# Performance work log

Hardware: AMD Instinct MI355X
Metric: run time of the kernel (lower is better)

The kernel has to match this reference:

```python
import jax, jax.numpy as jnp
import numpy as np

N = 100000   # nodes
E = 1600000  # edges
D = 128      # feature dim
G = 64       # graphs in batch


def setup_inputs() -> dict:
    key = jax.random.key(0)
    k1, k2, k3, k4, k5, k6, k7, k8 = jax.random.split(key, 8)
    in_feat = jax.random.normal(k1, (N, D), dtype=jnp.float32)
    src = jax.random.randint(k2, (E,), 0, N, dtype=jnp.int32)
    dst = jax.random.randint(k3, (E,), 0, N, dtype=jnp.int32)
    graph_ids = jax.random.randint(k4, (N,), 0, G, dtype=jnp.int32)
    s = 1.0 / np.sqrt(D)
    W1 = jax.random.uniform(k5, (D, D), jnp.float32, -s, s)
    b1 = jnp.zeros((D,), jnp.float32)
    W2 = jax.random.uniform(k6, (D, D), jnp.float32, -s, s)
    b2 = jnp.zeros((D,), jnp.float32)
    return {"in_feat": in_feat, "W1": W1, "b1": b1, "W2": W2, "b2": b2,
            "src": src, "dst": dst, "graph_ids": graph_ids}


def _graph_conv(x, src, dst, W, b, norm_src, norm_dst):
    # DGL GraphConv, norm='both': D_out^{-1/2} A D_in^{-1/2} X W + b
    m = (x * norm_src[:, None])[src]                       # [E, d] gather
    agg = jax.ops.segment_sum(m, dst, num_segments=N)      # [N, d] scatter-add
    return (agg * norm_dst[:, None]) @ W + b


def reference(in_feat, W1, b1, W2, b2, src, dst, graph_ids):
    ones_e = jnp.ones((E,), jnp.float32)
    deg_out = jax.ops.segment_sum(ones_e, src, num_segments=N)
    deg_in = jax.ops.segment_sum(ones_e, dst, num_segments=N)
    norm_src = jnp.where(deg_out > 0, deg_out, 1.0) ** -0.5  # D_out^{-1/2}
    norm_dst = jnp.where(deg_in > 0, deg_in, 1.0) ** -0.5    # D_in^{-1/2}

    h = _graph_conv(in_feat, src, dst, W1, b1, norm_src, norm_dst)
    h = jax.nn.relu(h)
    h = _graph_conv(h, src, dst, W2, b2, norm_src, norm_dst)

    # AvgPooling: per-graph mean over nodes -> [G, D]
    sums = jax.ops.segment_sum(h, graph_ids, num_segments=G)
    counts = jax.ops.segment_sum(jnp.ones((N,), jnp.float32), graph_ids, num_segments=G)
    return sums / jnp.maximum(counts, 1.0)[:, None]
```

## Files before the change

kernel.cpp:

```cpp
#include <hip/hip_runtime.h>
#include <cstdint>


#define DD 128
#define PB 512
#define GB 384
#define KC 32
#define CHK 3200

typedef __attribute__((ext_vector_type(8))) short bf16x8;
typedef __attribute__((ext_vector_type(4))) float f32x4;
typedef __attribute__((ext_vector_type(2))) float f32x2;

__device__ __forceinline__ unsigned short f2bf(float f) {
  union { float f; unsigned u; } v; v.f = f;
  unsigned r = (v.u + 0x7fff + ((v.u >> 16) & 1)) >> 16;
  return (unsigned short)r;
}
__device__ __forceinline__ float bfhi(unsigned u) {
  union { unsigned u; float f; } v; v.u = u & 0xffff0000u; return v.f;
}
__device__ __forceinline__ float bflo(unsigned u) {
  union { unsigned u; float f; } v; v.u = u << 16; return v.f;
}
__device__ __forceinline__ unsigned char f2fp8(float f) {
  return (unsigned char)(__builtin_amdgcn_cvt_pk_fp8_f32(f, f, 0, false) & 0xff);
}

__global__ __launch_bounds__(256) void k_part1a(const int* __restrict__ src, const int* __restrict__ dst,
                                                const int* __restrict__ gid,
                                                unsigned* __restrict__ histD, unsigned* __restrict__ histS,
                                                int* __restrict__ gcnt, int E, int N, int G) {
  __shared__ unsigned hD[256], hS[256];
  __shared__ int h64[64];
  hD[threadIdx.x] = 0; hS[threadIdx.x] = 0;
  if (threadIdx.x < 64) h64[threadIdx.x] = 0;
  __syncthreads();
  int chunk = (E + gridDim.x - 1) / gridDim.x;
  int e0 = blockIdx.x * chunk, e1 = min(E, e0 + chunk);
  for (int e = e0 + threadIdx.x; e < e1; e += 256) {
    atomicAdd(&hD[(unsigned)dst[e] >> 9], 1u);
    atomicAdd(&hS[(unsigned)src[e] >> 9], 1u);
  }
  int stride = gridDim.x * 256;
  for (int i = blockIdx.x * 256 + threadIdx.x; i < N; i += stride)
    atomicAdd(&h64[gid[i]], 1);
  __syncthreads();
  histD[blockIdx.x * 256 + threadIdx.x] = hD[threadIdx.x];
  histS[blockIdx.x * 256 + threadIdx.x] = hS[threadIdx.x];
  if (threadIdx.x < (unsigned)G) {
    int v = h64[threadIdx.x];
    if (v) atomicAdd(&gcnt[threadIdx.x], v);
  }
}

__global__ __launch_bounds__(256) void k_pscanA(unsigned* __restrict__ histD, unsigned* __restrict__ histS,
                                                unsigned* __restrict__ tot) {
  __shared__ unsigned excl[PB], psc[256];
  int table = blockIdx.x >> 8, b = blockIdx.x & 255;
  unsigned* hist = table ? histS : histD;
  int t = threadIdx.x;
  unsigned s0 = hist[(2 * t) * 256 + b];
  unsigned s1 = hist[(2 * t + 1) * 256 + b];
  unsigned pr = s0 + s1;
  psc[t] = pr;
  __syncthreads();
  for (int off = 1; off < 256; off <<= 1) {
    unsigned x = (t >= off) ? psc[t - off] : 0;
    __syncthreads();
    psc[t] += x;
    __syncthreads();
  }
  unsigned pex = psc[t] - pr;
  excl[2 * t] = pex;
  excl[2 * t + 1] = pex + s0;
  __syncthreads();
  hist[(2 * t) * 256 + b] = excl[2 * t];
  hist[(2 * t + 1) * 256 + b] = excl[2 * t + 1];
  if (t == 255) tot[table * 256 + b] = psc[255];
}

__global__ __launch_bounds__(256) void k_pscanB(const unsigned* __restrict__ tot,
                                                int* __restrict__ bsD, int* __restrict__ bsS) {
  __shared__ unsigned s[256];
  int t = threadIdx.x;
#pragma unroll
  for (int table = 0; table < 2; ++table) {
    int* bs = table ? bsS : bsD;
    unsigned v = tot[table * 256 + t];
    s[t] = v;
    __syncthreads();
    for (int off = 1; off < 256; off <<= 1) {
      unsigned x = (t >= off) ? s[t - off] : 0;
      __syncthreads();
      s[t] += x;
      __syncthreads();
    }
    bs[t] = (int)(s[t] - v);
    if (t == 255) bs[256] = (int)s[255];
    __syncthreads();
  }
}

__global__ __launch_bounds__(256) void k_pscanC(unsigned* __restrict__ histD, unsigned* __restrict__ histS,
                                                const int* __restrict__ bsD, const int* __restrict__ bsS) {
  int table = blockIdx.x >> 9, i = blockIdx.x & (PB - 1);
  unsigned* hist = table ? histS : histD;
  const int* bs = table ? bsS : bsD;
  hist[i * 256 + threadIdx.x] += (unsigned)bs[threadIdx.x];
}

__global__ __launch_bounds__(256) void k_part1c(const int* __restrict__ src, const int* __restrict__ dst,
                                                const unsigned* __restrict__ histD, const unsigned* __restrict__ histS,
                                                unsigned* __restrict__ pairD, unsigned* __restrict__ pairS, int E) {
  __shared__ unsigned pk[CHK];
  __shared__ unsigned char bk[CHK];
  __shared__ unsigned hist[256], cur[256], gbase[256], psc[256];
  int chunk = (E + gridDim.x - 1) / gridDim.x;
  int e0 = blockIdx.x * chunk, e1 = min(E, e0 + chunk);
  int n = e1 - e0;
  int t = threadIdx.x;
#pragma unroll
  for (int table = 0; table < 2; ++table) {
    const unsigned* gcur = (table ? histS : histD) + blockIdx.x * 256;
    unsigned* out = table ? pairS : pairD;
    hist[t] = 0;
    __syncthreads();
    for (int i = t; i < n; i += 256) {
      unsigned key = (unsigned)(table ? src[e0 + i] : dst[e0 + i]);
      atomicAdd(&hist[key >> 9], 1u);
    }
    __syncthreads();
    unsigned v = hist[t];
    psc[t] = v;
    __syncthreads();
    for (int off = 1; off < 256; off <<= 1) {
      unsigned x = (t >= off) ? psc[t - off] : 0;
      __syncthreads();
      psc[t] += x;
      __syncthreads();
    }
    unsigned excl = psc[t] - v;
    cur[t] = excl;
    gbase[t] = gcur[t] - excl;
    __syncthreads();
    for (int i = t; i < n; i += 256) {
      unsigned sv = (unsigned)src[e0 + i], dv = (unsigned)dst[e0 + i];
      unsigned key = table ? sv : dv;
      unsigned val = table ? (((sv & 511u) << 17) | dv) : (((dv & 511u) << 17) | sv);
      unsigned b = key >> 9;
      unsigned p = atomicAdd(&cur[b], 1u);
      pk[p] = val;
      bk[p] = (unsigned char)b;
    }
    __syncthreads();
    for (int i = t; i < n; i += 256)
      out[gbase[bk[i]] + i] = pk[i];
    __syncthreads();
  }
}

__global__ __launch_bounds__(256) void k_part2d(const unsigned* __restrict__ pairD, const int* __restrict__ bsD,
                                                int* __restrict__ offs, int* __restrict__ degI,
                                                int* __restrict__ srcS, int N) {
  __shared__ unsigned hist[512], excl[512], psc[256];
  int k = blockIdx.x, base = k << 9;
  int b0 = bsD[k], b1 = bsD[k + 1];
  hist[threadIdx.x] = 0; hist[threadIdx.x + 256] = 0;
  __syncthreads();
  for (int i = b0 + threadIdx.x; i < b1; i += 256)
    atomicAdd(&hist[pairD[i] >> 17], 1u);
  __syncthreads();
  unsigned s0 = hist[2 * threadIdx.x], s1 = hist[2 * threadIdx.x + 1];
  unsigned pr = s0 + s1;
  psc[threadIdx.x] = pr;
  __syncthreads();
  for (int off = 1; off < 256; off <<= 1) {
    unsigned x = (threadIdx.x >= off) ? psc[threadIdx.x - off] : 0;
    __syncthreads();
    psc[threadIdx.x] += x;
    __syncthreads();
  }
  unsigned pex = psc[threadIdx.x] - pr;
  excl[2 * threadIdx.x] = pex;
  excl[2 * threadIdx.x + 1] = pex + s0;
  __syncthreads();
  for (int j = threadIdx.x; j < 512; j += 256) {
    int node = base + j;
    if (node <= N) offs[node] = b0 + (int)excl[j];
    if (node < N) degI[node] = (int)hist[j];
  }
  __syncthreads();
  for (int i = b0 + threadIdx.x; i < b1; i += 256) {
    unsigned pkv = pairD[i];
    unsigned pos = atomicAdd(&excl[pkv >> 17], 1u);
    srcS[b0 + (int)pos] = (int)(pkv & 0x1FFFFu);
  }
}

__global__ __launch_bounds__(256) void k_norm(const int* __restrict__ degI, const int* __restrict__ gcnt,
                                              const int* __restrict__ gid,
                                              float* __restrict__ ndst, uint2* __restrict__ pwg, int N) {
  int i = blockIdx.x * blockDim.x + threadIdx.x;
  if (i >= N) return;
  float gi = (float)degI[i]; gi = gi > 0.f ? gi : 1.f;
  float nd = rsqrtf(gi);
  ndst[i] = nd;
  float c = (float)gcnt[gid[i]]; c = c > 1.f ? c : 1.f;
  float w = nd / c;
  union { float f; unsigned u; } v; v.f = w;
  pwg[i] = make_uint2(v.u, (unsigned)gid[i]);
}

__global__ __launch_bounds__(1024, 1) void k_pw(const unsigned* __restrict__ pairS, const int* __restrict__ bsS,
                                                const uint2* __restrict__ pwg,
                                                unsigned short* __restrict__ P16,
                                                float* __restrict__ nsrc, int N) {
  __shared__ float tile[512 * 64];
  __shared__ unsigned hist[512];
  int k = blockIdx.x, base = k << 9;
  int b0 = bsS[k], b1 = bsS[k + 1];
  for (int i = threadIdx.x; i < 512 * 64; i += 1024) tile[i] = 0.f;
  if (threadIdx.x < 512) hist[threadIdx.x] = 0;
  __syncthreads();
  for (int i = b0 + threadIdx.x; i < b1; i += 1024) {
    unsigned pkv = pairS[i];
    unsigned dv = pkv & 0x1FFFFu;
    unsigned sloc = pkv >> 17;
    atomicAdd(&hist[sloc], 1u);
    uint2 u = pwg[dv];
    union { unsigned u; float f; } w; w.u = u.x;
    atomicAdd(&tile[sloc * 64 + u.y], w.f);
  }
  __syncthreads();
  if (threadIdx.x < 512) {
    int node = base + threadIdx.x;
    if (node < N) {
      float g = (float)hist[threadIdx.x]; g = g > 0.f ? g : 1.f;
      nsrc[node] = rsqrtf(g);
    }
  }
  for (int grp = threadIdx.x; grp < 4096; grp += 1024) {
    int qb = grp >> 6, g = grp & 63;
    unsigned w0 = (unsigned)f2bf(tile[(qb * 8 + 0) * 64 + g]) | ((unsigned)f2bf(tile[(qb * 8 + 1) * 64 + g]) << 16);
    unsigned w1 = (unsigned)f2bf(tile[(qb * 8 + 2) * 64 + g]) | ((unsigned)f2bf(tile[(qb * 8 + 3) * 64 + g]) << 16);
    unsigned w2 = (unsigned)f2bf(tile[(qb * 8 + 4) * 64 + g]) | ((unsigned)f2bf(tile[(qb * 8 + 5) * 64 + g]) << 16);
    unsigned w3 = (unsigned)f2bf(tile[(qb * 8 + 6) * 64 + g]) | ((unsigned)f2bf(tile[(qb * 8 + 7) * 64 + g]) << 16);
    uint4 o = make_uint4(w0, w1, w2, w3);
    *(uint4*)(P16 + ((size_t)(base >> 3) + qb) * 512 + g * 8) = o;
  }
}

__global__ __launch_bounds__(128) void k_wprep(const float* __restrict__ W, unsigned short* __restrict__ Wt) {
  int n = blockIdx.x, k = threadIdx.x;
  Wt[n * 128 + k] = f2bf(W[k * 128 + n]);
}

__global__ __launch_bounds__(256) void k_gemm1(const float* __restrict__ X, const unsigned short* __restrict__ Wt,
                                               const float* __restrict__ nsrc,
                                               unsigned char* __restrict__ Z8, int N) {
  int wave = threadIdx.x >> 6, lane = threadIdx.x & 63;
  int quad = lane >> 4, l16 = lane & 15;
  int row0 = blockIdx.x * 64 + wave * 16;
  int arow = row0 + l16; if (arow >= N) arow = N - 1;
  const float* xr = X + (size_t)arow * 128 + quad * 8;
  f32x4 acc[8];
#pragma unroll
  for (int i = 0; i < 8; ++i) acc[i] = (f32x4){0.f, 0.f, 0.f, 0.f};
#pragma unroll
  for (int kb = 0; kb < 128; kb += 32) {
    float4 x0 = *(const float4*)(xr + kb);
    float4 x1 = *(const float4*)(xr + kb + 4);
    bf16x8 a;
    a[0] = (short)f2bf(x0.x); a[1] = (short)f2bf(x0.y);
    a[2] = (short)f2bf(x0.z); a[3] = (short)f2bf(x0.w);
    a[4] = (short)f2bf(x1.x); a[5] = (short)f2bf(x1.y);
    a[6] = (short)f2bf(x1.z); a[7] = (short)f2bf(x1.w);
#pragma unroll
    for (int nt = 0; nt < 8; ++nt) {
      bf16x8 b = *(const bf16x8*)(Wt + (size_t)(nt * 16 + l16) * 128 + kb + quad * 8);
      acc[nt] = __builtin_amdgcn_mfma_f32_16x16x32_bf16(a, b, acc[nt], 0, 0, 0);
    }
  }
  int rbase = row0 + quad * 4;
#pragma unroll
  for (int r = 0; r < 4; ++r) {
    int row = rbase + r;
    if (row < N) {
      float s = nsrc[row];
#pragma unroll
      for (int nt = 0; nt < 8; ++nt)
        Z8[(size_t)row * 128 + nt * 16 + l16] = f2fp8(acc[nt][r] * s);
    }
  }
}

#define ACCP(u) do {                                              \
    c0 += __builtin_amdgcn_cvt_pk_f32_fp8((u).x, false);          \
    c1 += __builtin_amdgcn_cvt_pk_f32_fp8((u).x, true);           \
    c2 += __builtin_amdgcn_cvt_pk_f32_fp8((u).y, false);          \
    c3 += __builtin_amdgcn_cvt_pk_f32_fp8((u).y, true);           \
  } while (0)

__global__ __launch_bounds__(256) void k_layer1(const unsigned char* __restrict__ Z8,
                                                const int* __restrict__ offs, const int* __restrict__ srcS,
                                                const float* __restrict__ b1,
                                                const float* __restrict__ nsrc, const float* __restrict__ ndst,
                                                unsigned short* __restrict__ Hb, int N) {
  int lane = threadIdx.x & 63;
  int q = lane >> 4, l16 = lane & 15;
  int d = blockIdx.x * 16 + (threadIdx.x >> 6) * 4 + q;
  bool live = d < N;
  int dc = live ? d : N - 1;
  int start = offs[dc];
  int end = live ? offs[dc + 1] : start;
  const int boff = l16 * 8;
  const unsigned char* zb = Z8 + boff;
  float4 bv0 = *(const float4*)(b1 + boff);
  float4 bv1 = *(const float4*)(b1 + boff + 4);
  float nd = ndst[dc], ns = nsrc[dc];
  f32x2 c0 = {0.f, 0.f}, c1 = {0.f, 0.f}, c2 = {0.f, 0.f}, c3 = {0.f, 0.f};
  int e = start;
  int rem = end - start;
  int s0 = (rem > 0) ? srcS[e] : 0;
  int s1 = (rem > 1) ? srcS[e + 1] : 0;
  while (__any(rem > 0)) {
    uint2 u0 = make_uint2(0u, 0u), u1 = make_uint2(0u, 0u);
    if (rem > 0) u0 = *(const uint2*)(zb + ((size_t)s0 << 7));
    if (rem > 1) u1 = *(const uint2*)(zb + ((size_t)s1 << 7));
    int rem2 = rem - 2;
    if (rem2 > 0) {
      s0 = srcS[e + 2];
      if (rem2 > 1) s1 = srcS[e + 3];
    }
    ACCP(u0);
    ACCP(u1);
    e += 2;
    rem = rem2;
  }
  if (live) {
    float h0 = fmaxf(fmaf(nd, c0[0], bv0.x), 0.f) * ns;
    float h1 = fmaxf(fmaf(nd, c0[1], bv0.y), 0.f) * ns;
    float h2 = fmaxf(fmaf(nd, c1[0], bv0.z), 0.f) * ns;
    float h3 = fmaxf(fmaf(nd, c1[1], bv0.w), 0.f) * ns;
    float h4 = fmaxf(fmaf(nd, c2[0], bv1.x), 0.f) * ns;
    float h5 = fmaxf(fmaf(nd, c2[1], bv1.y), 0.f) * ns;
    float h6 = fmaxf(fmaf(nd, c3[0], bv1.z), 0.f) * ns;
    float h7 = fmaxf(fmaf(nd, c3[1], bv1.w), 0.f) * ns;
    unsigned w0 = (unsigned)f2bf(h0) | ((unsigned)f2bf(h1) << 16);
    unsigned w1 = (unsigned)f2bf(h2) | ((unsigned)f2bf(h3) << 16);
    unsigned w2 = (unsigned)f2bf(h4) | ((unsigned)f2bf(h5) << 16);
    unsigned w3 = (unsigned)f2bf(h6) | ((unsigned)f2bf(h7) << 16);
    *(uint4*)(Hb + (size_t)d * 128 + boff) = make_uint4(w0, w1, w2, w3);
  }
}

__global__ __launch_bounds__(256) void k_poolgemm(const unsigned short* __restrict__ P16,
                                                  const unsigned short* __restrict__ Hb,
                                                  float* __restrict__ part, int N, int Kpad, int chunk) {
  __shared__ unsigned short Hl[KC * 128];
  int t = threadIdx.x;
  int r0 = blockIdx.x * chunk;
  int r1 = min(Kpad, r0 + chunk);
  int wv = t >> 6, lane = t & 63, quad = lane >> 4, l16 = lane & 15;
  f32x4 acc[8];
#pragma unroll
  for (int i = 0; i < 8; ++i) acc[i] = (f32x4){0.f, 0.f, 0.f, 0.f};
  for (int rb = r0; rb < r1; rb += KC) {
    int r = t >> 3, c = (t & 7) * 16;
    int cs = c ^ ((r >> 3) * 16);
    int row = rb + r;
    if (row < N) {
      const uint4* srcp = (const uint4*)(Hb + (size_t)row * 128 + c);
      *(uint4*)(Hl + r * 128 + cs) = srcp[0];
      *(uint4*)(Hl + r * 128 + cs + 8) = srcp[1];
    } else {
      uint4 z = make_uint4(0, 0, 0, 0);
      *(uint4*)(Hl + r * 128 + cs) = z;
      *(uint4*)(Hl + r * 128 + cs + 8) = z;
    }
    __syncthreads();
    bf16x8 a = *(const bf16x8*)(P16 + ((size_t)(rb >> 3) + quad) * 512 + (wv * 16 + l16) * 8);
#pragma unroll
    for (int ft = 0; ft < 8; ++ft) {
      bf16x8 b;
#pragma unroll
      for (int j = 0; j < 8; ++j) {
        int rr = quad * 8 + j;
        b[j] = (short)Hl[rr * 128 + ((ft ^ (rr >> 3)) * 16) + l16];
      }
      acc[ft] = __builtin_amdgcn_mfma_f32_16x16x32_bf16(a, b, acc[ft], 0, 0, 0);
    }
    __syncthreads();
  }
  float* bp = part + (size_t)blockIdx.x * 64 * DD;
#pragma unroll
  for (int ft = 0; ft < 8; ++ft)
#pragma unroll
    for (int rg = 0; rg < 4; ++rg)
      bp[(wv * 16 + quad * 4 + rg) * DD + ft * 16 + l16] = acc[ft][rg];
}

__global__ __launch_bounds__(256) void k_fold(const float* __restrict__ part, float* __restrict__ pooled) {
  int tid = blockIdx.x * 256 + threadIdx.x;
  int o = tid & 8191, grp = tid >> 13;
  float s = 0.f;
  for (int k = grp; k < GB; k += 8) s += part[(size_t)k * 8192 + o];
  unsafeAtomicAdd(&pooled[o], s);
}

__global__ __launch_bounds__(128) void k_out(const float* __restrict__ pooled, const float* __restrict__ W2,
                                             const float* __restrict__ b2, float* __restrict__ out) {
  __shared__ float p[DD];
  int g = blockIdx.x, d = threadIdx.x;
  p[d] = pooled[g * DD + d];
  __syncthreads();
  float a = b2[d];
#pragma unroll 4
  for (int k = 0; k < DD; ++k) a = fmaf(p[k], W2[k * DD + d], a);
  out[g * DD + d] = a;
}

extern "C" void kernel_launch(void* const* d_in, const int* in_sizes, int n_in,
                              void* d_out, int out_size, void* d_ws, size_t ws_size,
                              hipStream_t stream) {
  const float* X  = (const float*)d_in[0];
  const float* W1 = (const float*)d_in[1];
  const float* b1 = (const float*)d_in[2];
  const float* W2 = (const float*)d_in[3];
  const float* b2 = (const float*)d_in[4];
  const int* src  = (const int*)d_in[5];
  const int* dst  = (const int*)d_in[6];
  const int* gid  = (const int*)d_in[7];
  int E = in_sizes[5];
  int N = in_sizes[7];
  int G = out_size / DD;
  int nb = (N >> 9) + 1;
  int Kpad = nb << 9;
  int chunk = ((Kpad + GB * KC - 1) / (GB * KC)) * KC;

  char* w = (char*)d_ws;
  size_t o = 0;
  auto carve = [&](size_t bytes) { char* p = w + o; o += (bytes + 255) & ~(size_t)255; return p; };
  int*   gcnt   = (int*)  carve((size_t)G * 4);
  float* pooled = (float*)carve((size_t)G * DD * 4);
  size_t zeroBytes = o;
  unsigned* histD = (unsigned*)carve((size_t)PB * 256 * 4);
  unsigned* histS = (unsigned*)carve((size_t)PB * 256 * 4);
  unsigned* tot   = (unsigned*)carve(512 * 4);
  int*   bsD    = (int*)  carve(257 * 4);
  int*   bsS    = (int*)  carve(257 * 4);
  unsigned* pairD = (unsigned*)carve((size_t)E * 4);
  unsigned* pairS = (unsigned*)carve((size_t)E * 4);
  int*   srcS   = (int*)  carve((size_t)E * 4);
  int*   offs   = (int*)  carve((size_t)(N + 1) * 4);
  int*   degI   = (int*)  carve((size_t)N * 4);
  float* nsrc   = (float*)carve((size_t)N * 4);
  float* ndst   = (float*)carve((size_t)N * 4);
  uint2* pwg    = (uint2*)carve((size_t)N * 8);
  unsigned short* Wt = (unsigned short*)carve(128 * 128 * 2);
  unsigned char*  Z8 = (unsigned char*)carve((size_t)N * DD);
  unsigned short* Hb = (unsigned short*)carve((size_t)N * DD * 2);
  unsigned short* P16 = (unsigned short*)carve((size_t)Kpad * 64 * 2);
  float* part   = (float*)pairD;

  hipMemsetAsync(d_ws, 0, zeroBytes, stream);

  k_part1a<<<PB, 256, 0, stream>>>(src, dst, gid, histD, histS, gcnt, E, N, G);
  k_pscanA<<<512, 256, 0, stream>>>(histD, histS, tot);
  k_pscanB<<<1, 256, 0, stream>>>(tot, bsD, bsS);
  k_pscanC<<<2 * PB, 256, 0, stream>>>(histD, histS, bsD, bsS);
  k_part1c<<<PB, 256, 0, stream>>>(src, dst, histD, histS, pairD, pairS, E);
  k_part2d<<<nb, 256, 0, stream>>>(pairD, bsD, offs, degI, srcS, N);
  k_norm<<<(N + 255) / 256, 256, 0, stream>>>(degI, gcnt, gid, ndst, pwg, N);
  k_pw<<<nb, 1024, 0, stream>>>(pairS, bsS, pwg, P16, nsrc, N);
  k_wprep<<<128, 128, 0, stream>>>(W1, Wt);
  k_gemm1<<<(N + 63) / 64, 256, 0, stream>>>(X, Wt, nsrc, Z8, N);
  k_layer1<<<(N + 15) / 16, 256, 0, stream>>>(Z8, offs, srcS, b1, nsrc, ndst, Hb, N);
  k_poolgemm<<<GB, 256, 0, stream>>>(P16, Hb, part, N, Kpad, chunk);
  k_fold<<<256, 256, 0, stream>>>(part, pooled);
  k_out<<<G, DD, 0, stream>>>(pooled, W2, b2, (float*)d_out);
}
```

Before: 298.7 us.

## Fuse norm into part2d, merge partition passes, deepen gather prefetch, drop fold kernel

k_part1c now reuses the per-block histograms saved by k_part1a instead of recounting, and scatters both dst- and src-keyed pairs in a single pass over the edges. The separate k_norm kernel is folded into k_part2d, which writes ndst and pwg directly from its local degree histogram. The layer-1 gather loop prefetches four source indices per step instead of two to keep more loads in flight. k_poolgemm atomically adds its partial results straight into pooled, which removes the partial buffer and the k_fold kernel. The costs are two extra histogram arrays, roughly doubled shared memory in k_part1c, and much more atomic traffic onto a small pooled array.

```diff
diff --git a/kernel.cpp b/kernel.cpp
--- a/kernel.cpp
+++ b/kernel.cpp
@@ -17,12 +17,6 @@
   unsigned r = (v.u + 0x7fff + ((v.u >> 16) & 1)) >> 16;
   return (unsigned short)r;
 }
-__device__ __forceinline__ float bfhi(unsigned u) {
-  union { unsigned u; float f; } v; v.u = u & 0xffff0000u; return v.f;
-}
-__device__ __forceinline__ float bflo(unsigned u) {
-  union { unsigned u; float f; } v; v.u = u << 16; return v.f;
-}
 __device__ __forceinline__ unsigned char f2fp8(float f) {
   return (unsigned char)(__builtin_amdgcn_cvt_pk_fp8_f32(f, f, 0, false) & 0xff);
 }
@@ -30,6 +24,7 @@
 __global__ __launch_bounds__(256) void k_part1a(const int* __restrict__ src, const int* __restrict__ dst,
                                                 const int* __restrict__ gid,
                                                 unsigned* __restrict__ histD, unsigned* __restrict__ histS,
+                                                unsigned* __restrict__ rawD, unsigned* __restrict__ rawS,
                                                 int* __restrict__ gcnt, int E, int N, int G) {
   __shared__ unsigned hD[256], hS[256];
   __shared__ int h64[64];
@@ -46,8 +41,11 @@
   for (int i = blockIdx.x * 256 + threadIdx.x; i < N; i += stride)
     atomicAdd(&h64[gid[i]], 1);
   __syncthreads();
-  histD[blockIdx.x * 256 + threadIdx.x] = hD[threadIdx.x];
-  histS[blockIdx.x * 256 + threadIdx.x] = hS[threadIdx.x];
+  unsigned vd = hD[threadIdx.x], vs = hS[threadIdx.x];
+  histD[blockIdx.x * 256 + threadIdx.x] = vd;
+  histS[blockIdx.x * 256 + threadIdx.x] = vs;
+  rawD[blockIdx.x * 256 + threadIdx.x] = vd;
+  rawS[blockIdx.x * 256 + threadIdx.x] = vs;
   if (threadIdx.x < (unsigned)G) {
     int v = h64[threadIdx.x];
     if (v) atomicAdd(&gcnt[threadIdx.x], v);
@@ -112,56 +110,62 @@
 
 __global__ __launch_bounds__(256) void k_part1c(const int* __restrict__ src, const int* __restrict__ dst,
                                                 const unsigned* __restrict__ histD, const unsigned* __restrict__ histS,
+                                                const unsigned* __restrict__ rawD, const unsigned* __restrict__ rawS,
                                                 unsigned* __restrict__ pairD, unsigned* __restrict__ pairS, int E) {
-  __shared__ unsigned pk[CHK];
-  __shared__ unsigned char bk[CHK];
-  __shared__ unsigned hist[256], cur[256], gbase[256], psc[256];
+  __shared__ unsigned pkD[CHK], pkS[CHK];
+  __shared__ unsigned char bkD[CHK], bkS[CHK];
+  __shared__ unsigned curD[256], curS[256], gbD[256], gbS[256], psc[256];
   int chunk = (E + gridDim.x - 1) / gridDim.x;
   int e0 = blockIdx.x * chunk, e1 = min(E, e0 + chunk);
   int n = e1 - e0;
   int t = threadIdx.x;
-#pragma unroll
-  for (int table = 0; table < 2; ++table) {
-    const unsigned* gcur = (table ? histS : histD) + blockIdx.x * 256;
-    unsigned* out = table ? pairS : pairD;
-    hist[t] = 0;
-    __syncthreads();
-    for (int i = t; i < n; i += 256) {
-      unsigned key = (unsigned)(table ? src[e0 + i] : dst[e0 + i]);
-      atomicAdd(&hist[key >> 9], 1u);
-    }
-    __syncthreads();
-    unsigned v = hist[t];
-    psc[t] = v;
-    __syncthreads();
-    for (int off = 1; off < 256; off <<= 1) {
-      unsigned x = (t >= off) ? psc[t - off] : 0;
-      __syncthreads();
-      psc[t] += x;
-      __syncthreads();
-    }
-    unsigned excl = psc[t] - v;
-    cur[t] = excl;
-    gbase[t] = gcur[t] - excl;
-    __syncthreads();
-    for (int i = t; i < n; i += 256) {
-      unsigned sv = (unsigned)src[e0 + i], dv = (unsigned)dst[e0 + i];
-      unsigned key = table ? sv : dv;
-      unsigned val = table ? (((sv & 511u) << 17) | dv) : (((dv & 511u) << 17) | sv);
-      unsigned b = key >> 9;
-      unsigned p = atomicAdd(&cur[b], 1u);
-      pk[p] = val;
-      bk[p] = (unsigned char)b;
-    }
-    __syncthreads();
-    for (int i = t; i < n; i += 256)
-      out[gbase[bk[i]] + i] = pk[i];
-    __syncthreads();
-  }
+  unsigned vD = rawD[blockIdx.x * 256 + t];
+  psc[t] = vD;
+  __syncthreads();
+  for (int off = 1; off < 256; off <<= 1) {
+    unsigned x = (t >= off) ? psc[t - off] : 0;
+    __syncthreads();
+    psc[t] += x;
+    __syncthreads();
+  }
+  unsigned exD = psc[t] - vD;
+  curD[t] = exD;
+  gbD[t] = histD[blockIdx.x * 256 + t] - exD;
+  __syncthreads();
+  unsigned vS = rawS[blockIdx.x * 256 + t];
+  psc[t] = vS;
+  __syncthreads();
+  for (int off = 1; off < 256; off <<= 1) {
+    unsigned x = (t >= off) ? psc[t - off] : 0;
+    __syncthreads();
+    psc[t] += x;
+    __syncthreads();
+  }
+  unsigned exS = psc[t] - vS;
+  curS[t] = exS;
+  gbS[t] = histS[blockIdx.x * 256 + t] - exS;
+  __syncthreads();
+  for (int i = t; i < n; i += 256) {
+    unsigned sv = (unsigned)src[e0 + i], dv = (unsigned)dst[e0 + i];
+    unsigned bD = dv >> 9, bS = sv >> 9;
+    unsigned pD = atomicAdd(&curD[bD], 1u);
+    pkD[pD] = ((dv & 511u) << 17) | sv;
+    bkD[pD] = (unsigned char)bD;
+    unsigned pS = atomicAdd(&curS[bS], 1u);
+    pkS[pS] = ((sv & 511u) << 17) | dv;
+    bkS[pS] = (unsigned char)bS;
+  }
+  __syncthreads();
+  for (int i = t; i < n; i += 256)
+    pairD[gbD[bkD[i]] + i] = pkD[i];
+  for (int i = t; i < n; i += 256)
+    pairS[gbS[bkS[i]] + i] = pkS[i];
 }
 
 __global__ __launch_bounds__(256) void k_part2d(const unsigned* __restrict__ pairD, const int* __restrict__ bsD,
-                                                int* __restrict__ offs, int* __restrict__ degI,
+                                                const int* __restrict__ gcnt, const int* __restrict__ gid,
+                                                int* __restrict__ offs, float* __restrict__ ndst,
+                                                uint2* __restrict__ pwg,
                                                 int* __restrict__ srcS, int N) {
   __shared__ unsigned hist[512], excl[512], psc[256];
   int k = blockIdx.x, base = k << 9;
@@ -188,7 +192,15 @@
   for (int j = threadIdx.x; j < 512; j += 256) {
     int node = base + j;
     if (node <= N) offs[node] = b0 + (int)excl[j];
-    if (node < N) degI[node] = (int)hist[j];
+    if (node < N) {
+      float gi = (float)hist[j]; gi = gi > 0.f ? gi : 1.f;
+      float nd = rsqrtf(gi);
+      ndst[node] = nd;
+      float c = (float)gcnt[gid[node]]; c = c > 1.f ? c : 1.f;
+      float w = nd / c;
+      union { float f; unsigned u; } v; v.f = w;
+      pwg[node] = make_uint2(v.u, (unsigned)gid[node]);
+    }
   }
   __syncthreads();
   for (int i = b0 + threadIdx.x; i < b1; i += 256) {
@@ -196,20 +208,6 @@
     unsigned pos = atomicAdd(&excl[pkv >> 17], 1u);
     srcS[b0 + (int)pos] = (int)(pkv & 0x1FFFFu);
   }
-}
-
-__global__ __launch_bounds__(256) void k_norm(const int* __restrict__ degI, const int* __restrict__ gcnt,
-                                              const int* __restrict__ gid,
-                                              float* __restrict__ ndst, uint2* __restrict__ pwg, int N) {
-  int i = blockIdx.x * blockDim.x + threadIdx.x;
-  if (i >= N) return;
-  float gi = (float)degI[i]; gi = gi > 0.f ? gi : 1.f;
-  float nd = rsqrtf(gi);
-  ndst[i] = nd;
-  float c = (float)gcnt[gid[i]]; c = c > 1.f ? c : 1.f;
-  float w = nd / c;
-  union { float f; unsigned u; } v; v.f = w;
-  pwg[i] = make_uint2(v.u, (unsigned)gid[i]);
 }
 
 __global__ __launch_bounds__(1024, 1) void k_pw(const unsigned* __restrict__ pairS, const int* __restrict__ bsS,
@@ -322,21 +320,28 @@
   f32x2 c0 = {0.f, 0.f}, c1 = {0.f, 0.f}, c2 = {0.f, 0.f}, c3 = {0.f, 0.f};
   int e = start;
   int rem = end - start;
-  int s0 = (rem > 0) ? srcS[e] : 0;
-  int s1 = (rem > 1) ? srcS[e + 1] : 0;
+  int s0 = 0, s1 = 0, s2 = 0, s3 = 0;
+  if (rem > 0) s0 = srcS[e];
+  if (rem > 1) s1 = srcS[e + 1];
+  if (rem > 2) s2 = srcS[e + 2];
+  if (rem > 3) s3 = srcS[e + 3];
   while (__any(rem > 0)) {
     uint2 u0 = make_uint2(0u, 0u), u1 = make_uint2(0u, 0u);
+    uint2 u2 = make_uint2(0u, 0u), u3 = make_uint2(0u, 0u);
     if (rem > 0) u0 = *(const uint2*)(zb + ((size_t)s0 << 7));
     if (rem > 1) u1 = *(const uint2*)(zb + ((size_t)s1 << 7));
-    int rem2 = rem - 2;
-    if (rem2 > 0) {
-      s0 = srcS[e + 2];
-      if (rem2 > 1) s1 = srcS[e + 3];
-    }
+    if (rem > 2) u2 = *(const uint2*)(zb + ((size_t)s2 << 7));
+    if (rem > 3) u3 = *(const uint2*)(zb + ((size_t)s3 << 7));
+    if (rem > 4) s0 = srcS[e + 4];
+    if (rem > 5) s1 = srcS[e + 5];
+    if (rem > 6) s2 = srcS[e + 6];
+    if (rem > 7) s3 = srcS[e + 7];
     ACCP(u0);
     ACCP(u1);
-    e += 2;
-    rem = rem2;
+    ACCP(u2);
+    ACCP(u3);
+    e += 4;
+    rem -= 4;
   }
   if (live) {
     float h0 = fmaxf(fmaf(nd, c0[0], bv0.x), 0.f) * ns;
@@ -357,7 +362,7 @@
 
 __global__ __launch_bounds__(256) void k_poolgemm(const unsigned short* __restrict__ P16,
                                                   const unsigned short* __restrict__ Hb,
-                                                  float* __restrict__ part, int N, int Kpad, int chunk) {
+                                                  float* __restrict__ pooled, int N, int Kpad, int chunk) {
   __shared__ unsigned short Hl[KC * 128];
   int t = threadIdx.x;
   int r0 = blockIdx.x * chunk;
@@ -393,20 +398,11 @@
     }
     __syncthreads();
   }
-  float* bp = part + (size_t)blockIdx.x * 64 * DD;
 #pragma unroll
   for (int ft = 0; ft < 8; ++ft)
 #pragma unroll
     for (int rg = 0; rg < 4; ++rg)
-      bp[(wv * 16 + quad * 4 + rg) * DD + ft * 16 + l16] = acc[ft][rg];
-}
-
-__global__ __launch_bounds__(256) void k_fold(const float* __restrict__ part, float* __restrict__ pooled) {
-  int tid = blockIdx.x * 256 + threadIdx.x;
-  int o = tid & 8191, grp = tid >> 13;
-  float s = 0.f;
-  for (int k = grp; k < GB; k += 8) s += part[(size_t)k * 8192 + o];
-  unsafeAtomicAdd(&pooled[o], s);
+      unsafeAtomicAdd(&pooled[(wv * 16 + quad * 4 + rg) * DD + ft * 16 + l16], acc[ft][rg]);
 }
 
 __global__ __launch_bounds__(128) void k_out(const float* __restrict__ pooled, const float* __restrict__ W2,
@@ -447,6 +443,8 @@
   size_t zeroBytes = o;
   unsigned* histD = (unsigned*)carve((size_t)PB * 256 * 4);
   unsigned* histS = (unsigned*)carve((size_t)PB * 256 * 4);
+  unsigned* rawD  = (unsigned*)carve((size_t)PB * 256 * 4);
+  unsigned* rawS  = (unsigned*)carve((size_t)PB * 256 * 4);
   unsigned* tot   = (unsigned*)carve(512 * 4);
   int*   bsD    = (int*)  carve(257 * 4);
   int*   bsS    = (int*)  carve(257 * 4);
@@ -454,7 +452,6 @@
   unsigned* pairS = (unsigned*)carve((size_t)E * 4);
   int*   srcS   = (int*)  carve((size_t)E * 4);
   int*   offs   = (int*)  carve((size_t)(N + 1) * 4);
-  int*   degI   = (int*)  carve((size_t)N * 4);
   float* nsrc   = (float*)carve((size_t)N * 4);
   float* ndst   = (float*)carve((size_t)N * 4);
   uint2* pwg    = (uint2*)carve((size_t)N * 8);
@@ -462,22 +459,19 @@
   unsigned char*  Z8 = (unsigned char*)carve((size_t)N * DD);
   unsigned short* Hb = (unsigned short*)carve((size_t)N * DD * 2);
   unsigned short* P16 = (unsigned short*)carve((size_t)Kpad * 64 * 2);
-  float* part   = (float*)pairD;
 
   hipMemsetAsync(d_ws, 0, zeroBytes, stream);
 
-  k_part1a<<<PB, 256, 0, stream>>>(src, dst, gid, histD, histS, gcnt, E, N, G);
+  k_part1a<<<PB, 256, 0, stream>>>(src, dst, gid, histD, histS, rawD, rawS, gcnt, E, N, G);
   k_pscanA<<<512, 256, 0, stream>>>(histD, histS, tot);
   k_pscanB<<<1, 256, 0, stream>>>(tot, bsD, bsS);
   k_pscanC<<<2 * PB, 256, 0, stream>>>(histD, histS, bsD, bsS);
-  k_part1c<<<PB, 256, 0, stream>>>(src, dst, histD, histS, pairD, pairS, E);
-  k_part2d<<<nb, 256, 0, stream>>>(pairD, bsD, offs, degI, srcS, N);
-  k_norm<<<(N + 255) / 256, 256, 0, stream>>>(degI, gcnt, gid, ndst, pwg, N);
+  k_part1c<<<PB, 256, 0, stream>>>(src, dst, histD, histS, rawD, rawS, pairD, pairS, E);
+  k_part2d<<<nb, 256, 0, stream>>>(pairD, bsD, gcnt, gid, offs, ndst, pwg, srcS, N);
   k_pw<<<nb, 1024, 0, stream>>>(pairS, bsS, pwg, P16, nsrc, N);
   k_wprep<<<128, 128, 0, stream>>>(W1, Wt);
   k_gemm1<<<(N + 63) / 64, 256, 0, stream>>>(X, Wt, nsrc, Z8, N);
   k_layer1<<<(N + 15) / 16, 256, 0, stream>>>(Z8, offs, srcS, b1, nsrc, ndst, Hb, N);
-  k_poolgemm<<<GB, 256, 0, stream>>>(P16, Hb, part, N, Kpad, chunk);
-  k_fold<<<256, 256, 0, stream>>>(part, pooled);
+  k_poolgemm<<<GB, 256, 0, stream>>>(P16, Hb, pooled, N, Kpad, chunk);
   k_out<<<G, DD, 0, stream>>>(pooled, W2, b2, (float*)d_out);
 }
```

Measured after the change: 291.8 us. 1.02x faster.
